# Optimization experiments

Hardware: AMD Instinct MI355X
Metric: run time of the kernel (lower is better)

## Reference

```python
import jax, jax.numpy as jnp
import numpy as np

NUM_RELATION = 500
NUM_ENTITY = 100000
EMBED_DIM = 64
B, N = 8192, 128
MASK_BIG = 1e19


def setup_inputs() -> dict:
    key = jax.random.key(0)
    k1, k2, k3, k4, k5, k6, k7, k8 = jax.random.split(key, 8)
    inp = {
        "input": jax.random.normal(k1, (B, N, EMBED_DIM), dtype=jnp.float32),
        "neighbor": jax.random.randint(k2, (B, N, 2), 0, NUM_ENTITY + 1, dtype=jnp.int64),
        "query_relation_id": jax.random.randint(k3, (B,), 0, 2 * NUM_RELATION, dtype=jnp.int64),
        "weight": jax.random.uniform(k4, (B, N, 2), dtype=jnp.float32),
        # learned parameters (xavier-normal-like init)
        "mlp_w_weight": jax.random.normal(k5, (NUM_ENTITY * 2 + 1, EMBED_DIM), dtype=jnp.float32) * 0.02,
        "qrel_weight": jax.random.normal(k6, (NUM_RELATION * 2, EMBED_DIM), dtype=jnp.float32) * 0.02,
        "att_w": jax.random.normal(k7, (EMBED_DIM * 2, EMBED_DIM * 2), dtype=jnp.float32) * 0.05,
        "att_v": jax.random.normal(k8, (1, EMBED_DIM * 2), dtype=jnp.float32) * 0.05,
    }
    return inp


def reference(input, neighbor, query_relation_id, weight, mlp_w_weight, qrel_weight, att_w, att_v):
    # neighbor channels: relation id (indexes mlp_w), entity id (indexes mask tables)
    input_relation = neighbor[:, :, 0]
    input_entity = neighbor[:, :, 1]

    r = mlp_w_weight[input_relation]                         # [B,N,D] gather
    # hyperplane transform: e - <e, r_hat> r_hat  (F.normalize with eps=1e-12)
    norm = jnp.maximum(jnp.linalg.norm(r, axis=2, keepdims=True), 1e-12)
    normed = r / norm
    transformed = input - jnp.sum(input * normed, axis=2, keepdims=True) * normed

    # mask_emb: 1 for real entities, 0 for padding entity (id == NUM_ENTITY)
    mask = (input_entity < NUM_ENTITY).astype(transformed.dtype)[:, :, None]
    transformed = transformed * mask

    query = qrel_weight[query_relation_id][:, None, :]       # [B,1,D]
    query = jnp.broadcast_to(query, (query.shape[0], transformed.shape[1], query.shape[2]))

    # MLP attention: tanh([q; t] W) . v
    hidden = jnp.tanh(jnp.concatenate([query, transformed], axis=2) @ att_w)  # [B,N,2D]
    attention_logit = jnp.sum(hidden * att_v[0], axis=2)      # [B,N]

    # mask_weight: subtract 1e19 at padding entities
    mask_logit = jnp.where(input_entity == NUM_ENTITY, jnp.float32(MASK_BIG), jnp.float32(0.0))
    attention_logit = attention_logit - mask_logit

    attention_weight = jax.nn.softmax(attention_logit, axis=1)
    attention_weight = attention_weight + weight[:, :, 0] / (weight[:, :, 1] + 1)

    output = jnp.sum(transformed * attention_weight[:, :, None], axis=1)  # [B,D]
    return output, attention_weight
```

## Files before the change

### kernel.cpp

```cpp
#include <hip/hip_runtime.h>
#include <hip/hip_bf16.h>

#define NB 8192
#define NE 100000

typedef __bf16 bf16x8 __attribute__((ext_vector_type(8)));
typedef __bf16 bf16x4 __attribute__((ext_vector_type(4)));
typedef float  f32x4  __attribute__((ext_vector_type(4)));

template<int C>
__device__ __forceinline__ float dpp_mov(float v) {
  return __int_as_float(__builtin_amdgcn_update_dpp(
      0, __float_as_int(v), C, 0xF, 0xF, true));
}

__device__ __forceinline__ float red16(float v) {
  v += dpp_mov<0xB1>(v);
  v += dpp_mov<0x4E>(v);
  v += dpp_mov<0x141>(v);
  v += dpp_mov<0x140>(v);
  return v;
}

__device__ __forceinline__ float swz_xor16(float v) {
  return __int_as_float(__builtin_amdgcn_ds_swizzle(__float_as_int(v), 0x401F));
}

__device__ __forceinline__ float fast_tanh(float x) {
  float e = __expf(-2.0f * fabsf(x));
  float t = (1.0f - e) * __builtin_amdgcn_rcpf(1.0f + e);
  return copysignf(t, x);
}

__global__ void prep_kernel(const float* __restrict__ att_w,
                            const float* __restrict__ qrel,
                            __bf16* __restrict__ wsf,
                            float*  __restrict__ qpart) {
  const int t = threadIdx.x;
  const int bid = blockIdx.x;
  if (bid == 0) {
    for (int i = t; i < 8192; i += 128) {
      int e  = i & 7;
      int l  = (i >> 3) & 63;
      int ks = (i >> 9) & 1;
      int tc = i >> 10;
      int k = ks * 32 + ((l >> 4) << 3) + e;
      int j = tc * 16 + (l & 15);
      wsf[i] = (__bf16)att_w[(64 + k) * 128 + j];
    }
  } else {
    int rid = bid - 1;
    float acc = 0.f;
    for (int k = 0; k < 64; ++k)
      acc += qrel[rid * 64 + k] * att_w[k * 128 + t];
    qpart[rid * 128 + t] = acc;
  }
}

__global__ __launch_bounds__(256, 4)
void attn_kernel(const float* __restrict__ inp,
                 const int*   __restrict__ nb,
                 const int*   __restrict__ qid_p,
                 const float* __restrict__ wgt,
                 const float* __restrict__ mlp,
                 const float* __restrict__ attv,
                 const __bf16* __restrict__ wsf,
                 const float* __restrict__ qpart_t,
                 float* __restrict__ out) {
  __shared__ __attribute__((aligned(16))) __bf16 T16[128][72];
  __shared__ float plog[128], mlog[128], awl[128];
  __shared__ float part[4][64];

  const int t    = threadIdx.x;
  const int lane = t & 63;
  const int w    = t >> 6;
  const int g    = lane >> 4;
  const int q    = lane & 15;
  const int b    = blockIdx.x;

  const int qid = qid_p[b];
  float qpv[8], vv[8];
#pragma unroll
  for (int tc = 0; tc < 8; ++tc) {
    qpv[tc] = qpart_t[qid * 128 + tc * 16 + q];
    vv[tc]  = attv[tc * 16 + q];
  }
  const int rown = w * 32 + (lane & 31);
  float2 w01 = reinterpret_cast<const float2*>(wgt)[(size_t)b * 128 + rown];
  const float wr = w01.x / (w01.y + 1.0f);

  {
    int2 re[8];
#pragma unroll
    for (int i = 0; i < 8; ++i) {
      int n = w * 32 + i * 4 + g;
      re[i] = *reinterpret_cast<const int2*>(&nb[((size_t)b * 128 + n) * 2]);
    }
#pragma unroll
    for (int i = 0; i < 8; ++i) {
      int n = w * 32 + i * 4 + g;
      f32x4 iv = *reinterpret_cast<const f32x4*>(&inp[((size_t)b * 128 + n) * 64 + q * 4]);
      f32x4 rv = *reinterpret_cast<const f32x4*>(&mlp[(size_t)re[i].x * 64 + q * 4]);
      float s1 = red16(rv[0]*rv[0] + rv[1]*rv[1] + rv[2]*rv[2] + rv[3]*rv[3]);
      float s2 = red16(iv[0]*rv[0] + iv[1]*rv[1] + iv[2]*rv[2] + iv[3]*rv[3]);
      float f  = s2 / fmaxf(s1, 1e-24f);
      float m  = (re[i].y >= NE) ? 0.0f : 1.0f;
      bf16x4 tv;
#pragma unroll
      for (int j = 0; j < 4; ++j) tv[j] = (__bf16)((iv[j] - f * rv[j]) * m);
      *reinterpret_cast<bf16x4*>(&T16[n][q * 4]) = tv;
      if (q == 0) mlog[n] = (re[i].y == NE) ? 1e19f : 0.0f;
    }
  }
  asm volatile("s_waitcnt lgkmcnt(0)" ::: "memory");

  bf16x8 af[2][2];
#pragma unroll
  for (int tr = 0; tr < 2; ++tr) {
    int row = w * 32 + tr * 16 + q;
    af[tr][0] = *reinterpret_cast<const bf16x8*>(&T16[row][g * 8]);
    af[tr][1] = *reinterpret_cast<const bf16x8*>(&T16[row][g * 8 + 32]);
  }
  float p[2][4] = {{0,0,0,0},{0,0,0,0}};
#pragma unroll
  for (int h = 0; h < 2; ++h) {
    f32x4 acc[2][4];
#pragma unroll
    for (int tc2 = 0; tc2 < 4; ++tc2) {
      float qv = qpv[h * 4 + tc2];
      acc[0][tc2] = f32x4{qv, qv, qv, qv};
      acc[1][tc2] = f32x4{qv, qv, qv, qv};
    }
#pragma unroll
    for (int tc2 = 0; tc2 < 4; ++tc2) {
      int tc = h * 4 + tc2;
      bf16x8 b0 = *reinterpret_cast<const bf16x8*>(wsf + ((tc * 2 + 0) * 64 + lane) * 8);
      bf16x8 b1 = *reinterpret_cast<const bf16x8*>(wsf + ((tc * 2 + 1) * 64 + lane) * 8);
      acc[0][tc2] = __builtin_amdgcn_mfma_f32_16x16x32_bf16(af[0][0], b0, acc[0][tc2], 0, 0, 0);
      acc[1][tc2] = __builtin_amdgcn_mfma_f32_16x16x32_bf16(af[1][0], b0, acc[1][tc2], 0, 0, 0);
      acc[0][tc2] = __builtin_amdgcn_mfma_f32_16x16x32_bf16(af[0][1], b1, acc[0][tc2], 0, 0, 0);
      acc[1][tc2] = __builtin_amdgcn_mfma_f32_16x16x32_bf16(af[1][1], b1, acc[1][tc2], 0, 0, 0);
    }
#pragma unroll
    for (int tr = 0; tr < 2; ++tr)
#pragma unroll
      for (int tc2 = 0; tc2 < 4; ++tc2) {
        float v = vv[h * 4 + tc2];
        p[tr][0] += fast_tanh(acc[tr][tc2][0]) * v;
        p[tr][1] += fast_tanh(acc[tr][tc2][1]) * v;
        p[tr][2] += fast_tanh(acc[tr][tc2][2]) * v;
        p[tr][3] += fast_tanh(acc[tr][tc2][3]) * v;
      }
  }
#pragma unroll
  for (int tr = 0; tr < 2; ++tr) {
    float p0 = red16(p[tr][0]), p1 = red16(p[tr][1]);
    float p2 = red16(p[tr][2]), p3 = red16(p[tr][3]);
    if (q == 0) {
      int row = w * 32 + tr * 16 + g * 4;
      plog[row + 0] = p0;
      plog[row + 1] = p1;
      plog[row + 2] = p2;
      plog[row + 3] = p3;
    }
  }
  __syncthreads();

  {
    float l0 = plog[lane]      - mlog[lane];
    float l1 = plog[lane + 64] - mlog[lane + 64];
    float m = fmaxf(l0, l1);
    m = fmaxf(m, __shfl_xor(m, 1, 64));
    m = fmaxf(m, __shfl_xor(m, 2, 64));
    m = fmaxf(m, __shfl_xor(m, 4, 64));
    m = fmaxf(m, __shfl_xor(m, 8, 64));
    m = fmaxf(m, __shfl_xor(m, 16, 64));
    m = fmaxf(m, __shfl_xor(m, 32, 64));
    float e0 = __expf(l0 - m), e1 = __expf(l1 - m);
    float s = e0 + e1;
    s += __shfl_xor(s, 1, 64);
    s += __shfl_xor(s, 2, 64);
    s += __shfl_xor(s, 4, 64);
    s += __shfl_xor(s, 8, 64);
    s += __shfl_xor(s, 16, 64);
    s += __shfl_xor(s, 32, 64);
    float inv = __builtin_amdgcn_rcpf(s) * (2.0f - s * __builtin_amdgcn_rcpf(s));
    float lg = plog[rown] - mlog[rown];
    float aw = __expf(lg - m) * inv + wr;
    if (lane < 32) {
      awl[rown] = aw;
      float* awout = out + (size_t)NB * 64;
      awout[(size_t)b * 128 + rown] = aw;
    }
  }
  asm volatile("s_waitcnt lgkmcnt(0)" ::: "memory");

  {
    f32x4 s4 = {0.f, 0.f, 0.f, 0.f};
#pragma unroll
    for (int i = 0; i < 8; ++i) {
      int n = w * 32 + i * 4 + g;
      bf16x4 tv = *reinterpret_cast<const bf16x4*>(&T16[n][q * 4]);
      float a = awl[n];
      s4[0] += (float)tv[0] * a;
      s4[1] += (float)tv[1] * a;
      s4[2] += (float)tv[2] * a;
      s4[3] += (float)tv[3] * a;
    }
#pragma unroll
    for (int c = 0; c < 4; ++c) {
      float v = s4[c];
      v += swz_xor16(v);
      v += __shfl_xor(v, 32, 64);
      s4[c] = v;
    }
    if (lane < 16) *reinterpret_cast<f32x4*>(&part[w][lane * 4]) = s4;
  }
  __syncthreads();
  if (t < 64)
    out[(size_t)b * 64 + t] = part[0][t] + part[1][t] + part[2][t] + part[3][t];
}

extern "C" void kernel_launch(void* const* d_in, const int* in_sizes, int n_in,
                              void* d_out, int out_size, void* d_ws, size_t ws_size,
                              hipStream_t stream) {
  const float* inp  = (const float*)d_in[0];
  const int*   nb   = (const int*)d_in[1];
  const int*   qid  = (const int*)d_in[2];
  const float* wgt  = (const float*)d_in[3];
  const float* mlp  = (const float*)d_in[4];
  const float* qrel = (const float*)d_in[5];
  const float* attw = (const float*)d_in[6];
  const float* attv = (const float*)d_in[7];
  float* out = (float*)d_out;

  __bf16* wsf   = (__bf16*)d_ws;
  float*  qpart = (float*)((char*)d_ws + 16384);

  prep_kernel<<<1001, 128, 0, stream>>>(attw, qrel, wsf, qpart);
  attn_kernel<<<NB, 256, 0, stream>>>(inp, nb, qid, wgt, mlp, attv, wsf, qpart, out);
}
```

Before: 475.7 us.

## Build MFMA A-fragments directly in registers, eliminating LDS staging of transformed rows

Each lane now loads its neighbor row's input and relation embedding directly in MFMA A-fragment layout and computes the hyperplane projection in registers, removing the T16 shared-memory tile and its write/read round trip. The final weighted sum reuses the bf16 fragments in registers with DPP reductions, and the padding-mask logits are recomputed from the neighbor ids instead of being kept in shared memory. This trades LDS traffic and a barrier-like wait for wider, less coalesced global loads per lane, extra neighbor-id reloads and more reductions.

```diff
diff --git a/kernel.cpp b/kernel.cpp
--- a/kernel.cpp
+++ b/kernel.cpp
@@ -67,60 +67,72 @@
                  const __bf16* __restrict__ wsf,
                  const float* __restrict__ qpart_t,
                  float* __restrict__ out) {
-  __shared__ __attribute__((aligned(16))) __bf16 T16[128][72];
-  __shared__ float plog[128], mlog[128], awl[128];
+  __shared__ float plog[128], awl[128];
   __shared__ float part[4][64];
 
   const int t    = threadIdx.x;
   const int lane = t & 63;
   const int w    = t >> 6;
-  const int g    = lane >> 4;
-  const int q    = lane & 15;
+  const int r    = lane & 15;
+  const int c    = lane >> 4;
   const int b    = blockIdx.x;
 
   const int qid = qid_p[b];
   float qpv[8], vv[8];
 #pragma unroll
   for (int tc = 0; tc < 8; ++tc) {
-    qpv[tc] = qpart_t[qid * 128 + tc * 16 + q];
-    vv[tc]  = attv[tc * 16 + q];
+    qpv[tc] = qpart_t[qid * 128 + tc * 16 + r];
+    vv[tc]  = attv[tc * 16 + r];
   }
   const int rown = w * 32 + (lane & 31);
   float2 w01 = reinterpret_cast<const float2*>(wgt)[(size_t)b * 128 + rown];
   const float wr = w01.x / (w01.y + 1.0f);
 
-  {
-    int2 re[8];
-#pragma unroll
-    for (int i = 0; i < 8; ++i) {
-      int n = w * 32 + i * 4 + g;
-      re[i] = *reinterpret_cast<const int2*>(&nb[((size_t)b * 128 + n) * 2]);
-    }
-#pragma unroll
-    for (int i = 0; i < 8; ++i) {
-      int n = w * 32 + i * 4 + g;
-      f32x4 iv = *reinterpret_cast<const f32x4*>(&inp[((size_t)b * 128 + n) * 64 + q * 4]);
-      f32x4 rv = *reinterpret_cast<const f32x4*>(&mlp[(size_t)re[i].x * 64 + q * 4]);
-      float s1 = red16(rv[0]*rv[0] + rv[1]*rv[1] + rv[2]*rv[2] + rv[3]*rv[3]);
-      float s2 = red16(iv[0]*rv[0] + iv[1]*rv[1] + iv[2]*rv[2] + iv[3]*rv[3]);
-      float f  = s2 / fmaxf(s1, 1e-24f);
-      float m  = (re[i].y >= NE) ? 0.0f : 1.0f;
-      bf16x4 tv;
-#pragma unroll
-      for (int j = 0; j < 4; ++j) tv[j] = (__bf16)((iv[j] - f * rv[j]) * m);
-      *reinterpret_cast<bf16x4*>(&T16[n][q * 4]) = tv;
-      if (q == 0) mlog[n] = (re[i].y == NE) ? 1e19f : 0.0f;
-    }
-  }
-  asm volatile("s_waitcnt lgkmcnt(0)" ::: "memory");
-
   bf16x8 af[2][2];
+  int2 re[2];
 #pragma unroll
   for (int tr = 0; tr < 2; ++tr) {
-    int row = w * 32 + tr * 16 + q;
-    af[tr][0] = *reinterpret_cast<const bf16x8*>(&T16[row][g * 8]);
-    af[tr][1] = *reinterpret_cast<const bf16x8*>(&T16[row][g * 8 + 32]);
-  }
+    int n = w * 32 + tr * 16 + r;
+    re[tr] = *reinterpret_cast<const int2*>(&nb[((size_t)b * 128 + n) * 2]);
+  }
+#pragma unroll
+  for (int tr = 0; tr < 2; ++tr) {
+    int n = w * 32 + tr * 16 + r;
+    const float* iptr = &inp[((size_t)b * 128 + n) * 64 + c * 8];
+    f32x4 iv0 = *reinterpret_cast<const f32x4*>(iptr);
+    f32x4 iv1 = *reinterpret_cast<const f32x4*>(iptr + 4);
+    f32x4 iv2 = *reinterpret_cast<const f32x4*>(iptr + 32);
+    f32x4 iv3 = *reinterpret_cast<const f32x4*>(iptr + 36);
+    const float* rptr = &mlp[(size_t)re[tr].x * 64 + c * 8];
+    f32x4 rv0 = *reinterpret_cast<const f32x4*>(rptr);
+    f32x4 rv1 = *reinterpret_cast<const f32x4*>(rptr + 4);
+    f32x4 rv2 = *reinterpret_cast<const f32x4*>(rptr + 32);
+    f32x4 rv3 = *reinterpret_cast<const f32x4*>(rptr + 36);
+    float s1 = rv0[0]*rv0[0] + rv0[1]*rv0[1] + rv0[2]*rv0[2] + rv0[3]*rv0[3]
+             + rv1[0]*rv1[0] + rv1[1]*rv1[1] + rv1[2]*rv1[2] + rv1[3]*rv1[3]
+             + rv2[0]*rv2[0] + rv2[1]*rv2[1] + rv2[2]*rv2[2] + rv2[3]*rv2[3]
+             + rv3[0]*rv3[0] + rv3[1]*rv3[1] + rv3[2]*rv3[2] + rv3[3]*rv3[3];
+    float s2 = iv0[0]*rv0[0] + iv0[1]*rv0[1] + iv0[2]*rv0[2] + iv0[3]*rv0[3]
+             + iv1[0]*rv1[0] + iv1[1]*rv1[1] + iv1[2]*rv1[2] + iv1[3]*rv1[3]
+             + iv2[0]*rv2[0] + iv2[1]*rv2[1] + iv2[2]*rv2[2] + iv2[3]*rv2[3]
+             + iv3[0]*rv3[0] + iv3[1]*rv3[1] + iv3[2]*rv3[2] + iv3[3]*rv3[3];
+    s1 += swz_xor16(s1);  s2 += swz_xor16(s2);
+    s1 += __shfl_xor(s1, 32, 64);
+    s2 += __shfl_xor(s2, 32, 64);
+    float f   = s2 / fmaxf(s1, 1e-24f);
+    float msk = (re[tr].y >= NE) ? 0.0f : 1.0f;
+    bf16x8 a0, a1;
+#pragma unroll
+    for (int j = 0; j < 4; ++j) {
+      a0[j]     = (__bf16)((iv0[j] - f * rv0[j]) * msk);
+      a0[j + 4] = (__bf16)((iv1[j] - f * rv1[j]) * msk);
+      a1[j]     = (__bf16)((iv2[j] - f * rv2[j]) * msk);
+      a1[j + 4] = (__bf16)((iv3[j] - f * rv3[j]) * msk);
+    }
+    af[tr][0] = a0;
+    af[tr][1] = a1;
+  }
+
   float p[2][4] = {{0,0,0,0},{0,0,0,0}};
 #pragma unroll
   for (int h = 0; h < 2; ++h) {
@@ -156,8 +168,8 @@
   for (int tr = 0; tr < 2; ++tr) {
     float p0 = red16(p[tr][0]), p1 = red16(p[tr][1]);
     float p2 = red16(p[tr][2]), p3 = red16(p[tr][3]);
-    if (q == 0) {
-      int row = w * 32 + tr * 16 + g * 4;
+    if (r == 0) {
+      int row = w * 32 + tr * 16 + c * 4;
       plog[row + 0] = p0;
       plog[row + 1] = p1;
       plog[row + 2] = p2;
@@ -167,8 +179,10 @@
   __syncthreads();
 
   {
-    float l0 = plog[lane]      - mlog[lane];
-    float l1 = plog[lane + 64] - mlog[lane + 64];
+    int e0i = nb[((size_t)b * 128 + lane) * 2 + 1];
+    int e1i = nb[((size_t)b * 128 + lane + 64) * 2 + 1];
+    float l0 = plog[lane]      - ((e0i == NE) ? 1e19f : 0.0f);
+    float l1 = plog[lane + 64] - ((e1i == NE) ? 1e19f : 0.0f);
     float m = fmaxf(l0, l1);
     m = fmaxf(m, __shfl_xor(m, 1, 64));
     m = fmaxf(m, __shfl_xor(m, 2, 64));
@@ -184,37 +198,43 @@
     s += __shfl_xor(s, 8, 64);
     s += __shfl_xor(s, 16, 64);
     s += __shfl_xor(s, 32, 64);
-    float inv = __builtin_amdgcn_rcpf(s) * (2.0f - s * __builtin_amdgcn_rcpf(s));
-    float lg = plog[rown] - mlog[rown];
-    float aw = __expf(lg - m) * inv + wr;
+    float rcp = __builtin_amdgcn_rcpf(s);
+    float inv = rcp * (2.0f - s * rcp);
     if (lane < 32) {
+      int eri = nb[((size_t)b * 128 + rown) * 2 + 1];
+      float lg = plog[rown] - ((eri == NE) ? 1e19f : 0.0f);
+      float aw = __expf(lg - m) * inv + wr;
       awl[rown] = aw;
       float* awout = out + (size_t)NB * 64;
       awout[(size_t)b * 128 + rown] = aw;
     }
   }
-  asm volatile("s_waitcnt lgkmcnt(0)" ::: "memory");
 
   {
-    f32x4 s4 = {0.f, 0.f, 0.f, 0.f};
-#pragma unroll
-    for (int i = 0; i < 8; ++i) {
-      int n = w * 32 + i * 4 + g;
-      bf16x4 tv = *reinterpret_cast<const bf16x4*>(&T16[n][q * 4]);
-      float a = awl[n];
-      s4[0] += (float)tv[0] * a;
-      s4[1] += (float)tv[1] * a;
-      s4[2] += (float)tv[2] * a;
-      s4[3] += (float)tv[3] * a;
-    }
-#pragma unroll
-    for (int c = 0; c < 4; ++c) {
-      float v = s4[c];
-      v += swz_xor16(v);
-      v += __shfl_xor(v, 32, 64);
-      s4[c] = v;
-    }
-    if (lane < 16) *reinterpret_cast<f32x4*>(&part[w][lane * 4]) = s4;
+    float po0[8] = {0,0,0,0,0,0,0,0};
+    float po1[8] = {0,0,0,0,0,0,0,0};
+#pragma unroll
+    for (int tr = 0; tr < 2; ++tr) {
+      float a = awl[w * 32 + tr * 16 + r];
+      bf16x8 a0 = af[tr][0], a1 = af[tr][1];
+#pragma unroll
+      for (int e = 0; e < 8; ++e) {
+        po0[e] += (float)a0[e] * a;
+        po1[e] += (float)a1[e] * a;
+      }
+    }
+#pragma unroll
+    for (int e = 0; e < 8; ++e) {
+      po0[e] = red16(po0[e]);
+      po1[e] = red16(po1[e]);
+    }
+    if (r == 0) {
+#pragma unroll
+      for (int e = 0; e < 8; ++e) {
+        part[w][c * 8 + e]      = po0[e];
+        part[w][32 + c * 8 + e] = po1[e];
+      }
+    }
   }
   __syncthreads();
   if (t < 64)
```

After: 458.7 us. 3.6% less time.
